# Kernel optimization log

Hardware: AMD Instinct MI355X
Metric: run time of the kernel (lower is better)

## Reference

```python
import jax, jax.numpy as jnp
jax.config.update("jax_enable_x64", True)
import numpy as np

VOXEL_SIZE = 0.1   # size_scheduler.value
VBITS = 12         # bits per voxel coordinate (signed, offset by VOFF)
VMASK = (1 << VBITS) - 1
VOFF = 1 << (VBITS - 1)
GBITS = 10         # bits for group index (G=1024)


def setup_inputs() -> dict:
    key = jax.random.key(0)
    B, G, P, F = 64, 1024, 64, 3
    active_pred = jax.random.normal(key, (B * G, P, F), dtype=jnp.float32)
    active_mask = jnp.ones((B, G), dtype=bool)  # all active -> static nonzero count
    return {"active_pred": active_pred, "active_mask": active_mask}


def reference(active_pred, active_mask):
    N, P, F = active_pred.shape
    # active_mask.nonzero() -> [N, 2] (batch, group) ids
    bi, gi = jnp.nonzero(active_mask, size=N)
    bg = jnp.stack([bi, gi], axis=1).astype(jnp.int64)              # [N, 2]
    bg = jnp.broadcast_to(bg[:, None, :], (N, P, 2)).reshape(-1, 2)  # [N*P, 2]
    offsets = active_pred.reshape(-1, F)[:, :3]                      # [N*P, 3]
    vox = jnp.floor(offsets / VOXEL_SIZE).astype(jnp.int64)          # [N*P, 3]
    # Pack (b, g, vx, vy, vz) into one int64 key; packing is lexicographic-order
    # preserving, so sorted-unique of codes == torch.unique(dim=0) row order.
    v = vox + VOFF                                                   # nonnegative
    code = ((((bg[:, 0] << GBITS) | bg[:, 1]) << (3 * VBITS))
            | (v[:, 0] << (2 * VBITS)) | (v[:, 1] << VBITS) | v[:, 2])
    ucode, cluster_indices = jnp.unique(
        code, return_inverse=True, size=code.shape[0], fill_value=jnp.max(code))
    # Decode unique codes back to [U, 5] keys (padded tail repeats max key).
    ub = ucode >> (3 * VBITS + GBITS)
    ug = (ucode >> (3 * VBITS)) & ((1 << GBITS) - 1)
    uv0 = ((ucode >> (2 * VBITS)) & VMASK) - VOFF
    uv1 = ((ucode >> VBITS) & VMASK) - VOFF
    uv2 = (ucode & VMASK) - VOFF
    unique_keys = jnp.stack([ub, ug, uv0, uv1, uv2], axis=1)
    return unique_keys, cluster_indices
```

## Files before the change

### kernel.cpp

```cpp
#include <hip/hip_runtime.h>
#include <cstdint>

typedef unsigned long long u64;
typedef unsigned int u32;

constexpr int VBITS = 12;
constexpr int VOFF  = 1 << (VBITS - 1);
constexpr int GBITS = 10;

constexpr int GPB = 16;
constexpr int WPB = 4;
constexpr int GPW = 4;

__device__ inline u32 partner_xor(u32 k, int j) {
    switch (j) {
    case 1:  return (u32)__builtin_amdgcn_mov_dpp((int)k, 0xB1, 0xF, 0xF, true);
    case 2:  return (u32)__builtin_amdgcn_mov_dpp((int)k, 0x4E, 0xF, 0xF, true);
    case 4:  return (u32)__builtin_amdgcn_ds_swizzle((int)k, 0x101F);
    case 8:  return (u32)__builtin_amdgcn_ds_swizzle((int)k, 0x201F);
    case 16: return (u32)__builtin_amdgcn_ds_swizzle((int)k, 0x401F);
    default: return (u32)__shfl_xor((int)k, 32, 64);
    }
}

__device__ inline u32 wave_sort_u32(u32 k, int lane) {
    #pragma unroll
    for (int ks = 2; ks <= 64; ks <<= 1) {
        #pragma unroll
        for (int j = ks >> 1; j >= 1; j >>= 1) {
            u32 other = partner_xor(k, j);
            bool takeMin = ((lane & ks) == 0) == ((lane & j) == 0);
            u32 mn = min(k, other), mx = max(k, other);
            k = takeMin ? mn : mx;
        }
    }
    return k;
}

__device__ inline u64 wave_sort_u64(u64 k, int lane) {
    #pragma unroll
    for (int ks = 2; ks <= 64; ks <<= 1) {
        #pragma unroll
        for (int j = ks >> 1; j >= 1; j >>= 1) {
            u64 other = __shfl_xor(k, j, 64);
            bool takeMin = ((lane & ks) == 0) == ((lane & j) == 0);
            u64 mn = k < other ? k : other;
            u64 mx = k < other ? other : k;
            k = takeMin ? mn : mx;
        }
    }
    return k;
}

__device__ inline u32 lane_push(int dest_lane, u32 src) {
    return (u32)__builtin_amdgcn_ds_permute(dest_lane << 2, (int)src);
}

__global__ __launch_bounds__(256) void vox_build(
    const float* __restrict__ pred,
    u32* __restrict__ arr,
    u64* __restrict__ meta,
    u32* __restrict__ blockSums,
    int ngroups)
{
    __shared__ float sf[GPB * 192];
    __shared__ u32 s_ws[WPB];
    const int t = threadIdx.x, w = t >> 6, lane = t & 63, b = blockIdx.x;

    {
        const float4* p4 = (const float4*)pred + (size_t)b * (GPB * 48);
        const size_t f4tot = (size_t)ngroups * 48;
        float4* s4 = (float4*)sf;
        #pragma unroll
        for (int i = 0; i < 3; i++) {
            int idx = t + i * 256;
            if ((size_t)b * (GPB * 48) + idx < f4tot) s4[idx] = p4[idx];
        }
    }
    __syncthreads();

    u32 wsum = 0;
    for (int j = 0; j < GPW; ++j) {
        int gi = w * GPW + j, gid = b * GPB + gi;
        if (gid < ngroups) {
            const float* q = sf + gi * 192 + lane * 3;
            int v0 = (int)floorf(q[0] / 0.1f) + VOFF;
            int v1 = (int)floorf(q[1] / 0.1f) + VOFF;
            int v2 = (int)floorf(q[2] / 0.1f) + VOFF;
            int r0 = __shfl(v0, 0, 64), r1 = __shfl(v1, 0, 64), r2 = __shfl(v2, 0, 64);
            int d0 = v0 - r0 + 128, d1 = v1 - r1 + 128, d2 = v2 - r2 + 128;
            bool bad = ((u32)(d0 | d1 | d2) > 255u) || ((u32)(v0 | v1 | v2) > 4095u);

            u32 cnt, packed;
            if (!__any(bad)) {
                u32 k = ((u32)d0 << 22) | ((u32)d1 << 14) | ((u32)d2 << 6) | (u32)lane;
                k = wave_sort_u32(k, lane);
                u32 sk = k >> 6;
                u32 pv = __shfl_up(sk, 1, 64);
                int flag = (lane == 0 || sk != pv) ? 1 : 0;
                u64 bal = __ballot(flag);
                int rank = (int)__popcll(bal & ((1ull << lane) - 1ull)) + flag - 1;
                cnt = (u32)__popcll(bal);
                int orig = (int)(k & 63);

                u32 dByRank = lane_push(rank, sk);
                u32 rByOrig = lane_push(orig, (u32)rank);
                packed = (dByRank & 0xFFFFFFu) | (rByOrig << 24);

                if (lane == 0)
                    meta[gid] = ((u64)((u32)(r0 - 128) & 4095))
                              | ((u64)((u32)(r1 - 128) & 4095) << 12)
                              | ((u64)((u32)(r2 - 128) & 4095) << 24)
                              | ((u64)cnt << 48);
            } else {
                u64 code = ((u64)(long long)v0 << 24) | ((u64)(long long)v1 << 12)
                         | (u64)(long long)v2;
                u64 k = wave_sort_u64((code << 6) | (u64)lane, lane);
                u64 sk = k >> 6, pv = __shfl_up(sk, 1, 64);
                int flag = (lane == 0 || sk != pv) ? 1 : 0;
                u64 bal = __ballot(flag);
                int rank = (int)__popcll(bal & ((1ull << lane) - 1ull)) + flag - 1;
                cnt = (u32)__popcll(bal);
                int orig = (int)(k & 63);
                u32 rByOrig = lane_push(orig, (u32)rank);
                packed = rByOrig << 24;
                if (lane == 0) meta[gid] = ((u64)cnt << 48) | (1ull << 56);
            }
            arr[(size_t)gid * 64 + lane] = packed;
            wsum += cnt;
        }
    }
    if (lane == 0) s_ws[w] = wsum;
    __syncthreads();
    if (t == 0) blockSums[b] = s_ws[0] + s_ws[1] + s_ws[2] + s_ws[3];
}

__global__ __launch_bounds__(256) void vox_emit(
    const float* __restrict__ pred,
    const u32* __restrict__ arr,
    const u64* __restrict__ meta,
    const u32* __restrict__ blockSums,
    int* __restrict__ okeys,
    int* __restrict__ inv,
    int ngroups, int totalrows, int nblocks)
{
    __shared__ u32 s_scr[512];
    __shared__ u32 s_c[GPB];
    __shared__ u32 s_baseU[2];
    __shared__ int s_tail[5];
    const int t = threadIdx.x, w = t >> 6, lane = t & 63, b = blockIdx.x;

    u32 a[GPW]; u64 m[GPW];
    #pragma unroll
    for (int j = 0; j < GPW; ++j) {
        int gid = b * GPB + w * GPW + j;
        if (gid < ngroups) {
            a[j] = arr[(size_t)gid * 64 + lane];
            m[j] = meta[gid];
        } else { a[j] = 0; m[j] = 0; }
    }

    if (t < GPB) {
        int gid = b * GPB + t;
        s_c[t] = (gid < ngroups) ? (u32)((meta[gid] >> 48) & 127) : 0;
    }

    {
        u32 below = 0, all = 0;
        for (int i = t; i < nblocks; i += 256) {
            u32 v = blockSums[i];
            all += v;
            if (i < b) below += v;
        }
        __syncthreads();
        s_scr[t] = below; s_scr[256 + t] = all;
        __syncthreads();
        #pragma unroll
        for (int off = 128; off >= 1; off >>= 1) {
            if (t < off) {
                s_scr[t]       += s_scr[t + off];
                s_scr[256 + t] += s_scr[256 + t + off];
            }
            __syncthreads();
        }
        if (t == 0) { s_baseU[0] = s_scr[0]; s_baseU[1] = s_scr[256]; }
        __syncthreads();
    }

    u32 base = s_baseU[0];
    #pragma unroll
    for (int i = 0; i < GPB; i++) if (i < w * GPW) base += s_c[i];

    #pragma unroll
    for (int j = 0; j < GPW; ++j) {
        int gid = b * GPB + w * GPW + j;
        if (gid < ngroups) {
            u32 cnt = (u32)((m[j] >> 48) & 127);
            u32 rinv = a[j] >> 24;

            inv[(size_t)gid * 64 + lane] = (int)(base + rinv);

            int vd0 = 0, vd1 = 0, vd2 = 0;
            if (!((m[j] >> 56) & 1)) {
                u32 d = a[j] & 0xFFFFFFu;
                u32 m0 = (u32)m[j] & 4095, m1 = (u32)(m[j] >> 12) & 4095,
                    m2 = (u32)(m[j] >> 24) & 4095;
                vd0 = (int)((m0 + ((d >> 16) & 255)) & 4095);
                vd1 = (int)((m1 + ((d >> 8) & 255)) & 4095);
                vd2 = (int)((m2 + (d & 255)) & 4095);
            } else {
                const float* p = pred + (size_t)gid * 192 + lane * 3;
                long long w0 = (long long)floorf(p[0] / 0.1f) + VOFF;
                long long w1 = (long long)floorf(p[1] / 0.1f) + VOFF;
                long long w2 = (long long)floorf(p[2] / 0.1f) + VOFF;
                u64 code = ((u64)w0 << 24) | ((u64)w1 << 12) | (u64)w2;
                u32 clo = (u32)__builtin_amdgcn_ds_permute((int)(rinv << 2), (int)(u32)code);
                u32 chi = (u32)__builtin_amdgcn_ds_permute((int)(rinv << 2), (int)(u32)(code >> 32));
                u64 c = ((u64)chi << 32) | clo;
                vd0 = (int)((c >> 24) & 4095);
                vd1 = (int)((c >> 12) & 4095);
                vd2 = (int)(c & 4095);
            }

            if (lane < (int)cnt) {
                int* dst = okeys + (size_t)(base + lane) * 5;
                dst[0] = gid >> GBITS;
                dst[1] = gid & ((1 << GBITS) - 1);
                dst[2] = vd0 - VOFF;
                dst[3] = vd1 - VOFF;
                dst[4] = vd2 - VOFF;
            }
            base += cnt;
        }
    }

    if (w == 0) {
        int lg = ngroups - 1;
        const float* p = pred + (size_t)lg * 192 + lane * 3;
        long long w0 = (long long)floorf(p[0] / 0.1f) + VOFF;
        long long w1 = (long long)floorf(p[1] / 0.1f) + VOFF;
        long long w2 = (long long)floorf(p[2] / 0.1f) + VOFF;
        u64 code = ((u64)w0 << 24) | ((u64)w1 << 12) | (u64)w2;
        #pragma unroll
        for (int off = 32; off >= 1; off >>= 1) {
            u64 o = __shfl_xor(code, off, 64);
            code = (o > code) ? o : code;
        }
        if (lane == 0) {
            s_tail[0] = lg >> GBITS;
            s_tail[1] = lg & ((1 << GBITS) - 1);
            s_tail[2] = (int)((code >> 24) & 4095) - VOFF;
            s_tail[3] = (int)((code >> 12) & 4095) - VOFF;
            s_tail[4] = (int)(code & 4095) - VOFF;
        }
    }
    __syncthreads();
    {
        u32 U = s_baseU[1];
        u32 total5 = (u32)totalrows * 5u;
        u32 stride = (u32)gridDim.x * 256u;
        for (u32 e = U * 5u + (u32)b * 256u + (u32)t; e < total5; e += stride)
            okeys[e] = s_tail[e % 5u];
    }
}

extern "C" void kernel_launch(void* const* d_in, const int* in_sizes, int n_in,
                              void* d_out, int out_size, void* d_ws, size_t ws_size,
                              hipStream_t stream)
{
    const float* pred = (const float*)d_in[0];
    int ngroups   = in_sizes[1];
    int totalrows = in_sizes[0] / 3;
    int nblocks   = (ngroups + GPB - 1) / GPB;

    int* okeys = (int*)d_out;
    int* inv   = okeys + (size_t)totalrows * 5;

    char* ws = (char*)d_ws;
    u64* meta      = (u64*)ws;
    u32* arr       = (u32*)(meta + ngroups);
    u32* blockSums = arr + (size_t)ngroups * 64;

    vox_build<<<nblocks, 256, 0, stream>>>(pred, arr, meta, blockSums, ngroups);
    vox_emit<<<nblocks, 256, 0, stream>>>(pred, arr, meta, blockSums,
                                          okeys, inv, ngroups, totalrows, nblocks);
}
```

Measured before the change: 54.42 us.

## Fuse build and emit kernels with decoupled look-back scan

Merges the two-kernel build/emit pipeline into one kernel that keeps the per-group sorted results and metadata in shared memory. A decoupled look-back scan over per-block tile descriptors in global memory replaces the separate blockSums pass. Blocks now cover 64 groups and read pred directly from global memory instead of staging it in shared memory. Only the last block fills the padded tail. This removes the workspace round trip and one launch, but adds a memset launch and serial look-back latency, and it relies on blocks making forward progress in launch order.

```diff
diff --git a/kernel.cpp b/kernel.cpp
--- a/kernel.cpp
+++ b/kernel.cpp
@@ -8,9 +8,11 @@
 constexpr int VOFF  = 1 << (VBITS - 1);
 constexpr int GBITS = 10;
 
-constexpr int GPB = 16;
-constexpr int WPB = 4;
-constexpr int GPW = 4;
+constexpr int GPB  = 64;
+constexpr int WPB  = 4;
+constexpr int CH   = 4;
+constexpr int CGP  = 16;
+constexpr int GPWC = 4;
 
 __device__ inline u32 partner_xor(u32 k, int j) {
     switch (j) {
@@ -56,210 +58,207 @@
     return (u32)__builtin_amdgcn_ds_permute(dest_lane << 2, (int)src);
 }
 
-__global__ __launch_bounds__(256) void vox_build(
+__device__ inline u32 wave_reduce_sum(u32 x) {
+    #pragma unroll
+    for (int off = 32; off >= 1; off >>= 1) x += __shfl_xor(x, off, 64);
+    return x;
+}
+
+__device__ inline u64 tile_load(const u64* p) {
+    return __hip_atomic_load(p, __ATOMIC_RELAXED, __HIP_MEMORY_SCOPE_AGENT);
+}
+__device__ inline void tile_store(u64* p, u64 v) {
+    __hip_atomic_store(p, v, __ATOMIC_RELAXED, __HIP_MEMORY_SCOPE_AGENT);
+}
+
+__global__ __launch_bounds__(256, 5) void vox_fused(
     const float* __restrict__ pred,
-    u32* __restrict__ arr,
-    u64* __restrict__ meta,
-    u32* __restrict__ blockSums,
-    int ngroups)
+    u64* __restrict__ tiles,
+    int* __restrict__ okeys,
+    int* __restrict__ inv,
+    int ngroups, int totalrows)
 {
-    __shared__ float sf[GPB * 192];
+    __shared__ u32 s_pk[GPB * 64];
+    __shared__ u64 s_meta[GPB];
+    __shared__ u32 s_c[GPB];
+    __shared__ u32 s_off[GPB];
     __shared__ u32 s_ws[WPB];
+    __shared__ u32 s_base[2];
+    __shared__ int s_tail[5];
+
     const int t = threadIdx.x, w = t >> 6, lane = t & 63, b = blockIdx.x;
 
-    {
-        const float4* p4 = (const float4*)pred + (size_t)b * (GPB * 48);
-        const size_t f4tot = (size_t)ngroups * 48;
-        float4* s4 = (float4*)sf;
-        #pragma unroll
-        for (int i = 0; i < 3; i++) {
-            int idx = t + i * 256;
-            if ((size_t)b * (GPB * 48) + idx < f4tot) s4[idx] = p4[idx];
-        }
-    }
-    __syncthreads();
-
     u32 wsum = 0;
-    for (int j = 0; j < GPW; ++j) {
-        int gi = w * GPW + j, gid = b * GPB + gi;
-        if (gid < ngroups) {
-            const float* q = sf + gi * 192 + lane * 3;
-            int v0 = (int)floorf(q[0] / 0.1f) + VOFF;
-            int v1 = (int)floorf(q[1] / 0.1f) + VOFF;
-            int v2 = (int)floorf(q[2] / 0.1f) + VOFF;
-            int r0 = __shfl(v0, 0, 64), r1 = __shfl(v1, 0, 64), r2 = __shfl(v2, 0, 64);
-            int d0 = v0 - r0 + 128, d1 = v1 - r1 + 128, d2 = v2 - r2 + 128;
-            bool bad = ((u32)(d0 | d1 | d2) > 255u) || ((u32)(v0 | v1 | v2) > 4095u);
-
-            u32 cnt, packed;
-            if (!__any(bad)) {
-                u32 k = ((u32)d0 << 22) | ((u32)d1 << 14) | ((u32)d2 << 6) | (u32)lane;
-                k = wave_sort_u32(k, lane);
-                u32 sk = k >> 6;
-                u32 pv = __shfl_up(sk, 1, 64);
-                int flag = (lane == 0 || sk != pv) ? 1 : 0;
-                u64 bal = __ballot(flag);
-                int rank = (int)__popcll(bal & ((1ull << lane) - 1ull)) + flag - 1;
-                cnt = (u32)__popcll(bal);
-                int orig = (int)(k & 63);
-
-                u32 dByRank = lane_push(rank, sk);
-                u32 rByOrig = lane_push(orig, (u32)rank);
-                packed = (dByRank & 0xFFFFFFu) | (rByOrig << 24);
-
-                if (lane == 0)
-                    meta[gid] = ((u64)((u32)(r0 - 128) & 4095))
-                              | ((u64)((u32)(r1 - 128) & 4095) << 12)
-                              | ((u64)((u32)(r2 - 128) & 4095) << 24)
-                              | ((u64)cnt << 48);
-            } else {
-                u64 code = ((u64)(long long)v0 << 24) | ((u64)(long long)v1 << 12)
-                         | (u64)(long long)v2;
-                u64 k = wave_sort_u64((code << 6) | (u64)lane, lane);
-                u64 sk = k >> 6, pv = __shfl_up(sk, 1, 64);
-                int flag = (lane == 0 || sk != pv) ? 1 : 0;
-                u64 bal = __ballot(flag);
-                int rank = (int)__popcll(bal & ((1ull << lane) - 1ull)) + flag - 1;
-                cnt = (u32)__popcll(bal);
-                int orig = (int)(k & 63);
-                u32 rByOrig = lane_push(orig, (u32)rank);
-                packed = rByOrig << 24;
-                if (lane == 0) meta[gid] = ((u64)cnt << 48) | (1ull << 56);
-            }
-            arr[(size_t)gid * 64 + lane] = packed;
-            wsum += cnt;
+    for (int c = 0; c < CH; ++c) {
+        for (int j = 0; j < GPWC; ++j) {
+            int idx = c * CGP + w * GPWC + j;
+            int gid = b * GPB + idx;
+            if (gid < ngroups) {
+                const float* q = pred + (size_t)gid * 192 + lane * 3;
+                int v0 = (int)floorf(q[0] / 0.1f) + VOFF;
+                int v1 = (int)floorf(q[1] / 0.1f) + VOFF;
+                int v2 = (int)floorf(q[2] / 0.1f) + VOFF;
+                int r0 = __shfl(v0, 0, 64), r1 = __shfl(v1, 0, 64), r2 = __shfl(v2, 0, 64);
+                int d0 = v0 - r0 + 128, d1 = v1 - r1 + 128, d2 = v2 - r2 + 128;
+                bool bad = ((u32)(d0 | d1 | d2) > 255u) || ((u32)(v0 | v1 | v2) > 4095u);
+
+                u32 cnt, packed;
+                if (!__any(bad)) {
+                    u32 k = ((u32)d0 << 22) | ((u32)d1 << 14) | ((u32)d2 << 6) | (u32)lane;
+                    k = wave_sort_u32(k, lane);
+                    u32 sk = k >> 6;
+                    u32 pv = __shfl_up(sk, 1, 64);
+                    int flag = (lane == 0 || sk != pv) ? 1 : 0;
+                    u64 bal = __ballot(flag);
+                    int rank = (int)__popcll(bal & ((1ull << lane) - 1ull)) + flag - 1;
+                    cnt = (u32)__popcll(bal);
+                    int orig = (int)(k & 63);
+
+                    u32 dByRank = lane_push(rank, sk);
+                    u32 rByOrig = lane_push(orig, (u32)rank);
+                    packed = (dByRank & 0xFFFFFFu) | (rByOrig << 24);
+
+                    if (lane == 0)
+                        s_meta[idx] = ((u64)((u32)(r0 - 128) & 4095))
+                                    | ((u64)((u32)(r1 - 128) & 4095) << 12)
+                                    | ((u64)((u32)(r2 - 128) & 4095) << 24)
+                                    | ((u64)cnt << 48);
+                } else {
+                    u64 code = ((u64)(long long)v0 << 24) | ((u64)(long long)v1 << 12)
+                             | (u64)(long long)v2;
+                    u64 k = wave_sort_u64((code << 6) | (u64)lane, lane);
+                    u64 sk = k >> 6, pv = __shfl_up(sk, 1, 64);
+                    int flag = (lane == 0 || sk != pv) ? 1 : 0;
+                    u64 bal = __ballot(flag);
+                    int rank = (int)__popcll(bal & ((1ull << lane) - 1ull)) + flag - 1;
+                    cnt = (u32)__popcll(bal);
+                    int orig = (int)(k & 63);
+                    u32 rByOrig = lane_push(orig, (u32)rank);
+                    packed = rByOrig << 24;
+                    if (lane == 0) s_meta[idx] = ((u64)cnt << 48) | (1ull << 56);
+                }
+                s_pk[idx * 64 + lane] = packed;
+                if (lane == 0) s_c[idx] = cnt;
+                wsum += cnt;
+            } else if (lane == 0) {
+                s_c[idx] = 0; s_meta[idx] = 0;
+            }
         }
     }
     if (lane == 0) s_ws[w] = wsum;
     __syncthreads();
-    if (t == 0) blockSums[b] = s_ws[0] + s_ws[1] + s_ws[2] + s_ws[3];
-}
-
-__global__ __launch_bounds__(256) void vox_emit(
-    const float* __restrict__ pred,
-    const u32* __restrict__ arr,
-    const u64* __restrict__ meta,
-    const u32* __restrict__ blockSums,
-    int* __restrict__ okeys,
-    int* __restrict__ inv,
-    int ngroups, int totalrows, int nblocks)
-{
-    __shared__ u32 s_scr[512];
-    __shared__ u32 s_c[GPB];
-    __shared__ u32 s_baseU[2];
-    __shared__ int s_tail[5];
-    const int t = threadIdx.x, w = t >> 6, lane = t & 63, b = blockIdx.x;
-
-    u32 a[GPW]; u64 m[GPW];
-    #pragma unroll
-    for (int j = 0; j < GPW; ++j) {
-        int gid = b * GPB + w * GPW + j;
-        if (gid < ngroups) {
-            a[j] = arr[(size_t)gid * 64 + lane];
-            m[j] = meta[gid];
-        } else { a[j] = 0; m[j] = 0; }
-    }
-
-    if (t < GPB) {
-        int gid = b * GPB + t;
-        s_c[t] = (gid < ngroups) ? (u32)((meta[gid] >> 48) & 127) : 0;
-    }
-
-    {
-        u32 below = 0, all = 0;
-        for (int i = t; i < nblocks; i += 256) {
-            u32 v = blockSums[i];
-            all += v;
-            if (i < b) below += v;
+
+    if (w == 0) {
+        u32 T = s_ws[0] + s_ws[1] + s_ws[2] + s_ws[3];
+        if (lane == 0) tile_store(&tiles[b], (1ull << 32) | (u64)T);
+
+        u32 x = s_c[lane];
+        u32 incl = x;
+        #pragma unroll
+        for (int off = 1; off < 64; off <<= 1) {
+            u32 v = __shfl_up(incl, off, 64);
+            if (lane >= off) incl += v;
+        }
+        s_off[lane] = incl - x;
+
+        u32 excl = 0;
+        int jb = b - 1;
+        while (true) {
+            int idx2 = jb - lane;
+            u64 v = (idx2 >= 0) ? tile_load(&tiles[idx2]) : (2ull << 32);
+            u32 st  = (u32)(v >> 32);
+            u32 val = (u32)v;
+            u64 pm = __ballot(st == 2);
+            int fp = pm ? (int)(__ffsll((unsigned long long)pm) - 1) : 64;
+            u64 im = __ballot(st == 0);
+            u64 before = (fp >= 64) ? ~0ull : ((1ull << fp) - 1ull);
+            if (im & before) continue;
+            u32 contrib = (lane <= fp) ? val : 0;
+            excl += wave_reduce_sum(contrib);
+            if (fp < 64) break;
+            jb -= 64;
+        }
+        if (lane == 0) {
+            tile_store(&tiles[b], (2ull << 32) | (u64)(excl + T));
+            s_base[0] = excl;
+            s_base[1] = excl + T;
+        }
+    }
+    __syncthreads();
+
+    const u32 baseAll = s_base[0];
+    for (int c = 0; c < CH; ++c) {
+        for (int j = 0; j < GPWC; ++j) {
+            int idx = c * CGP + w * GPWC + j;
+            int gid = b * GPB + idx;
+            if (gid < ngroups) {
+                u64 m  = s_meta[idx];
+                u32 a  = s_pk[idx * 64 + lane];
+                u32 cnt = (u32)((m >> 48) & 127);
+                u32 rinv = a >> 24;
+                u32 bg = baseAll + s_off[idx];
+
+                inv[(size_t)gid * 64 + lane] = (int)(bg + rinv);
+
+                int vd0 = 0, vd1 = 0, vd2 = 0;
+                if (!((m >> 56) & 1)) {
+                    u32 d = a & 0xFFFFFFu;
+                    u32 m0 = (u32)m & 4095, m1 = (u32)(m >> 12) & 4095,
+                        m2 = (u32)(m >> 24) & 4095;
+                    vd0 = (int)((m0 + ((d >> 16) & 255)) & 4095);
+                    vd1 = (int)((m1 + ((d >> 8) & 255)) & 4095);
+                    vd2 = (int)((m2 + (d & 255)) & 4095);
+                } else {
+                    const float* p = pred + (size_t)gid * 192 + lane * 3;
+                    long long w0 = (long long)floorf(p[0] / 0.1f) + VOFF;
+                    long long w1 = (long long)floorf(p[1] / 0.1f) + VOFF;
+                    long long w2 = (long long)floorf(p[2] / 0.1f) + VOFF;
+                    u64 code = ((u64)w0 << 24) | ((u64)w1 << 12) | (u64)w2;
+                    u32 clo = (u32)__builtin_amdgcn_ds_permute((int)(rinv << 2), (int)(u32)code);
+                    u32 chi = (u32)__builtin_amdgcn_ds_permute((int)(rinv << 2), (int)(u32)(code >> 32));
+                    u64 cc = ((u64)chi << 32) | clo;
+                    vd0 = (int)((cc >> 24) & 4095);
+                    vd1 = (int)((cc >> 12) & 4095);
+                    vd2 = (int)(cc & 4095);
+                }
+
+                if (lane < (int)cnt) {
+                    int* dst = okeys + (size_t)(bg + lane) * 5;
+                    dst[0] = gid >> GBITS;
+                    dst[1] = gid & ((1 << GBITS) - 1);
+                    dst[2] = vd0 - VOFF;
+                    dst[3] = vd1 - VOFF;
+                    dst[4] = vd2 - VOFF;
+                }
+            }
+        }
+    }
+
+    if (b == (int)gridDim.x - 1) {
+        if (w == 0) {
+            int lg = ngroups - 1;
+            const float* p = pred + (size_t)lg * 192 + lane * 3;
+            long long w0 = (long long)floorf(p[0] / 0.1f) + VOFF;
+            long long w1 = (long long)floorf(p[1] / 0.1f) + VOFF;
+            long long w2 = (long long)floorf(p[2] / 0.1f) + VOFF;
+            u64 code = ((u64)w0 << 24) | ((u64)w1 << 12) | (u64)w2;
+            #pragma unroll
+            for (int off = 32; off >= 1; off >>= 1) {
+                u64 o = __shfl_xor(code, off, 64);
+                code = (o > code) ? o : code;
+            }
+            if (lane == 0) {
+                s_tail[0] = lg >> GBITS;
+                s_tail[1] = lg & ((1 << GBITS) - 1);
+                s_tail[2] = (int)((code >> 24) & 4095) - VOFF;
+                s_tail[3] = (int)((code >> 12) & 4095) - VOFF;
+                s_tail[4] = (int)(code & 4095) - VOFF;
+            }
         }
         __syncthreads();
-        s_scr[t] = below; s_scr[256 + t] = all;
-        __syncthreads();
-        #pragma unroll
-        for (int off = 128; off >= 1; off >>= 1) {
-            if (t < off) {
-                s_scr[t]       += s_scr[t + off];
-                s_scr[256 + t] += s_scr[256 + t + off];
-            }
-            __syncthreads();
-        }
-        if (t == 0) { s_baseU[0] = s_scr[0]; s_baseU[1] = s_scr[256]; }
-        __syncthreads();
-    }
-
-    u32 base = s_baseU[0];
-    #pragma unroll
-    for (int i = 0; i < GPB; i++) if (i < w * GPW) base += s_c[i];
-
-    #pragma unroll
-    for (int j = 0; j < GPW; ++j) {
-        int gid = b * GPB + w * GPW + j;
-        if (gid < ngroups) {
-            u32 cnt = (u32)((m[j] >> 48) & 127);
-            u32 rinv = a[j] >> 24;
-
-            inv[(size_t)gid * 64 + lane] = (int)(base + rinv);
-
-            int vd0 = 0, vd1 = 0, vd2 = 0;
-            if (!((m[j] >> 56) & 1)) {
-                u32 d = a[j] & 0xFFFFFFu;
-                u32 m0 = (u32)m[j] & 4095, m1 = (u32)(m[j] >> 12) & 4095,
-                    m2 = (u32)(m[j] >> 24) & 4095;
-                vd0 = (int)((m0 + ((d >> 16) & 255)) & 4095);
-                vd1 = (int)((m1 + ((d >> 8) & 255)) & 4095);
-                vd2 = (int)((m2 + (d & 255)) & 4095);
-            } else {
-                const float* p = pred + (size_t)gid * 192 + lane * 3;
-                long long w0 = (long long)floorf(p[0] / 0.1f) + VOFF;
-                long long w1 = (long long)floorf(p[1] / 0.1f) + VOFF;
-                long long w2 = (long long)floorf(p[2] / 0.1f) + VOFF;
-                u64 code = ((u64)w0 << 24) | ((u64)w1 << 12) | (u64)w2;
-                u32 clo = (u32)__builtin_amdgcn_ds_permute((int)(rinv << 2), (int)(u32)code);
-                u32 chi = (u32)__builtin_amdgcn_ds_permute((int)(rinv << 2), (int)(u32)(code >> 32));
-                u64 c = ((u64)chi << 32) | clo;
-                vd0 = (int)((c >> 24) & 4095);
-                vd1 = (int)((c >> 12) & 4095);
-                vd2 = (int)(c & 4095);
-            }
-
-            if (lane < (int)cnt) {
-                int* dst = okeys + (size_t)(base + lane) * 5;
-                dst[0] = gid >> GBITS;
-                dst[1] = gid & ((1 << GBITS) - 1);
-                dst[2] = vd0 - VOFF;
-                dst[3] = vd1 - VOFF;
-                dst[4] = vd2 - VOFF;
-            }
-            base += cnt;
-        }
-    }
-
-    if (w == 0) {
-        int lg = ngroups - 1;
-        const float* p = pred + (size_t)lg * 192 + lane * 3;
-        long long w0 = (long long)floorf(p[0] / 0.1f) + VOFF;
-        long long w1 = (long long)floorf(p[1] / 0.1f) + VOFF;
-        long long w2 = (long long)floorf(p[2] / 0.1f) + VOFF;
-        u64 code = ((u64)w0 << 24) | ((u64)w1 << 12) | (u64)w2;
-        #pragma unroll
-        for (int off = 32; off >= 1; off >>= 1) {
-            u64 o = __shfl_xor(code, off, 64);
-            code = (o > code) ? o : code;
-        }
-        if (lane == 0) {
-            s_tail[0] = lg >> GBITS;
-            s_tail[1] = lg & ((1 << GBITS) - 1);
-            s_tail[2] = (int)((code >> 24) & 4095) - VOFF;
-            s_tail[3] = (int)((code >> 12) & 4095) - VOFF;
-            s_tail[4] = (int)(code & 4095) - VOFF;
-        }
-    }
-    __syncthreads();
-    {
-        u32 U = s_baseU[1];
+        u32 U = s_base[1];
         u32 total5 = (u32)totalrows * 5u;
-        u32 stride = (u32)gridDim.x * 256u;
-        for (u32 e = U * 5u + (u32)b * 256u + (u32)t; e < total5; e += stride)
+        for (u32 e = U * 5u + (u32)t; e < total5; e += 256u)
             okeys[e] = s_tail[e % 5u];
     }
 }
@@ -276,12 +275,9 @@
     int* okeys = (int*)d_out;
     int* inv   = okeys + (size_t)totalrows * 5;
 
-    char* ws = (char*)d_ws;
-    u64* meta      = (u64*)ws;
-    u32* arr       = (u32*)(meta + ngroups);
-    u32* blockSums = arr + (size_t)ngroups * 64;
-
-    vox_build<<<nblocks, 256, 0, stream>>>(pred, arr, meta, blockSums, ngroups);
-    vox_emit<<<nblocks, 256, 0, stream>>>(pred, arr, meta, blockSums,
-                                          okeys, inv, ngroups, totalrows, nblocks);
-}
+    u64* tiles = (u64*)d_ws;
+
+    hipMemsetAsync(tiles, 0, (size_t)nblocks * sizeof(u64), stream);
+    vox_fused<<<nblocks, 256, 0, stream>>>(pred, tiles, okeys, inv,
+                                           ngroups, totalrows);
+}
```

Result: slower. 56.83 us (+4.4%).
